# Kernel optimization log

Hardware: AMD Instinct MI355X
Metric: run time of the kernel (lower is better)

The kernel has to match this reference:

```python
import jax, jax.numpy as jnp
import numpy as np

C = 256  # image_channels == mask_channels == output_channels

def setup_inputs() -> dict:
    key = jax.random.key(0)
    ks = jax.random.split(key, 10)
    B, H, W = 16, 48, 48
    s = 0.02
    return {
        "image_feat": jax.random.normal(ks[0], (B, C, H, W), jnp.float32),
        "mask_feat": jax.random.normal(ks[1], (B, C, H, W), jnp.float32),
        "Wq": jax.random.normal(ks[2], (C, C), jnp.float32) * s,
        "bq": jnp.zeros((C,), jnp.float32),
        "Wk": jax.random.normal(ks[3], (C, C), jnp.float32) * s,
        "bk": jnp.zeros((C,), jnp.float32),
        "Wv": jax.random.normal(ks[4], (C, C), jnp.float32) * s,
        "bv": jnp.zeros((C,), jnp.float32),
        "Wo": jax.random.normal(ks[5], (C, C), jnp.float32) * s,
        "bo": jnp.zeros((C,), jnp.float32),
    }

def reference(image_feat, mask_feat, Wq, bq, Wk, bk, Wv, bv, Wo, bo):
    B, Cc, H, W = image_feat.shape
    N = H * W
    img = image_feat.reshape(B, Cc, N)   # [B, C, N]
    msk = mask_feat.reshape(B, Cc, N)
    # 1x1 convs == per-pixel linear over channels
    q = jnp.einsum('oc,bcn->bon', Wq, msk) + bq[None, :, None]
    k = jnp.einsum('oc,bcn->bon', Wk, img) + bk[None, :, None]
    v = jnp.einsum('oc,bcn->bon', Wv, img) + bv[None, :, None]
    scale = Cc ** (-0.5)
    # attn[b, n, m] = <q[:, n], k[:, m]>
    attn = jnp.einsum('bcn,bcm->bnm', q, k) * scale
    attn = jax.nn.softmax(attn, axis=-1)
    # attended[b, c, n] = sum_m v[b, c, m] * attn[b, n, m]
    av = jnp.einsum('bcm,bnm->bcn', v, attn)
    out = jnp.einsum('oc,bcn->bon', Wo, av) + bo[None, :, None]
    return image_feat + out.reshape(B, Cc, H, W)
```

## Files before the change

### kernel.cpp

```cpp
#include <hip/hip_runtime.h>

#define NBATCH 16
#define CCH 256
#define NTOK 2304

typedef __attribute__((ext_vector_type(8))) short bf16x8;
typedef __attribute__((ext_vector_type(4))) short bf16x4v;
typedef __attribute__((ext_vector_type(4))) float f32x4;

__device__ __forceinline__ short f2bf(float x){
  unsigned u = __builtin_bit_cast(unsigned, x);
  u = u + 0x7FFFu + ((u >> 16) & 1u);
  return (short)(u >> 16);
}
__device__ __forceinline__ float bf2f(short h){
  unsigned u = ((unsigned)(unsigned short)h) << 16;
  return __builtin_bit_cast(float, u);
}
__device__ __forceinline__ unsigned char f2fp8(float v){
  return (unsigned char)(__builtin_amdgcn_cvt_pk_fp8_f32(v, v, 0, false) & 0xff);
}

__device__ __forceinline__ void gld_lds16(const void* g, void* l){
  __builtin_amdgcn_global_load_lds((const __attribute__((address_space(1))) void*)g,
                                   (__attribute__((address_space(3))) void*)l, 16, 0, 0);
}

__global__ __launch_bounds__(256) void cw_kernel(const float* __restrict__ Wq, const float* __restrict__ Wk,
                                                 const float* __restrict__ Wv, const float* __restrict__ Wo,
                                                 short* __restrict__ out){
  int idx = blockIdx.x * 256 + threadIdx.x;
  int which = idx >> 14;
  int off = idx & 16383;
  const float* src = which==0 ? Wq : which==1 ? Wk : which==2 ? Wv : Wo;
  float4 v = ((const float4*)src)[off];
  bf16x4v pk = { f2bf(v.x), f2bf(v.y), f2bf(v.z), f2bf(v.w) };
  *(bf16x4v*)(out + ((size_t)which << 16) + ((size_t)off << 2)) = pk;
}

__global__ __launch_bounds__(256) void prep_kernel(const float* __restrict__ img, const float* __restrict__ msk,
                                                   short* __restrict__ imgT, short* __restrict__ mskT){
  int zz = blockIdx.z; int b = zz >> 1; int which = zz & 1;
  const float* src = (which ? msk : img) + (size_t)b * CCH * NTOK;
  short* dst = (which ? mskT : imgT) + (size_t)b * NTOK * CCH;
  int n0 = blockIdx.x * 64, c0 = blockIdx.y * 64;
  __shared__ __align__(16) short tile[64][72];
  int tid = threadIdx.x;
  int r = tid >> 2, g = tid & 3;
  const float* p = src + (size_t)(c0 + r) * NTOK + n0 + 16 * g;
  #pragma unroll
  for (int q4 = 0; q4 < 4; q4++){
    float4 v = *(const float4*)(p + 4 * q4);
    tile[16*g + 4*q4 + 0][r] = f2bf(v.x);
    tile[16*g + 4*q4 + 1][r] = f2bf(v.y);
    tile[16*g + 4*q4 + 2][r] = f2bf(v.z);
    tile[16*g + 4*q4 + 3][r] = f2bf(v.w);
  }
  __syncthreads();
  short* qp = dst + (size_t)(n0 + r) * CCH + c0 + 16 * g;
  *(bf16x8*)qp = *(const bf16x8*)&tile[r][16*g];
  *(bf16x8*)(qp + 8) = *(const bf16x8*)&tile[r][16*g + 8];
}

__device__ __forceinline__ void gemm128(const short* __restrict__ Ablk, const short* __restrict__ Bblk,
                                        short* As, short* Bs, f32x4 (&acc)[4][4]){
  const int tid = threadIdx.x;
  const int l = tid & 63, w = tid >> 6;
  const int l15 = l & 15, lhi = l >> 4;
  const int wi = w >> 1, wj = w & 1;
  const int srow = tid >> 3, scs = tid & 7;
  const f32x4 z4 = {0.f, 0.f, 0.f, 0.f};
  #pragma unroll
  for (int mt = 0; mt < 4; mt++)
    #pragma unroll
    for (int nt = 0; nt < 4; nt++) acc[mt][nt] = z4;

  #pragma unroll 1
  for (int kt = 0; kt < 4; kt++){
    const int k0 = kt * 64;
    bf16x8 ra[4], rb[4];
    #pragma unroll
    for (int p = 0; p < 4; p++){
      const int row = p * 32 + srow;
      ra[p] = *(const bf16x8*)(Ablk + (size_t)row * CCH + k0 + 8 * scs);
      rb[p] = *(const bf16x8*)(Bblk + (size_t)row * CCH + k0 + 8 * scs);
    }
    __syncthreads();
    #pragma unroll
    for (int p = 0; p < 4; p++){
      const int row = p * 32 + srow;
      const int sw = (scs ^ (row & 7)) << 3;
      *(bf16x8*)(As + row * 64 + sw) = ra[p];
      *(bf16x8*)(Bs + row * 64 + sw) = rb[p];
    }
    __syncthreads();
    #pragma unroll
    for (int kk = 0; kk < 2; kk++){
      bf16x8 afr[4], bfr[4];
      #pragma unroll
      for (int mt = 0; mt < 4; mt++){
        const int row = 64 * wi + 16 * mt + l15;
        const int ch = 4 * kk + lhi;
        afr[mt] = *(const bf16x8*)(As + row * 64 + ((ch ^ (row & 7)) << 3));
      }
      #pragma unroll
      for (int nt = 0; nt < 4; nt++){
        const int row = 64 * wj + 16 * nt + l15;
        const int ch = 4 * kk + lhi;
        bfr[nt] = *(const bf16x8*)(Bs + row * 64 + ((ch ^ (row & 7)) << 3));
      }
      #pragma unroll
      for (int mt = 0; mt < 4; mt++)
        #pragma unroll
        for (int nt = 0; nt < 4; nt++)
          acc[mt][nt] = __builtin_amdgcn_mfma_f32_16x16x32_bf16(afr[mt], bfr[nt], acc[mt][nt], 0, 0, 0);
    }
  }
}

__global__ __launch_bounds__(256) void proj_kernel(const short* __restrict__ imgT, const short* __restrict__ mskT,
                                                   const short* __restrict__ Wb,
                                                   const float* __restrict__ bq, const float* __restrict__ bk,
                                                   const float* __restrict__ bv,
                                                   unsigned char* __restrict__ Q8, unsigned char* __restrict__ K8,
                                                   short* __restrict__ Vn){
  __shared__ __align__(16) short As[128 * 64];
  __shared__ __align__(16) short Bs[128 * 64];
  const int b = blockIdx.z, which = blockIdx.y, bx = blockIdx.x;
  const size_t nbT = (size_t)b * NTOK * CCH;
  const short* Ablk; const short* Bblk; const float* bias;
  int ti, tj;
  if (which == 0){
    ti = bx >> 1; tj = bx & 1;
    Ablk = mskT + nbT + (size_t)ti * 128 * CCH;
    Bblk = Wb + (size_t)tj * 128 * CCH;
    bias = bq;
  } else if (which == 1){
    ti = bx >> 1; tj = bx & 1;
    Ablk = imgT + nbT + (size_t)ti * 128 * CCH;
    Bblk = Wb + 65536 + (size_t)tj * 128 * CCH;
    bias = bk;
  } else {
    ti = bx / 18; tj = bx % 18;
    Ablk = Wb + 2 * 65536 + (size_t)ti * 128 * CCH;
    Bblk = imgT + nbT + (size_t)tj * 128 * CCH;
    bias = bv;
  }
  f32x4 acc[4][4];
  gemm128(Ablk, Bblk, As, Bs, acc);
  const int l = threadIdx.x & 63, w = threadIdx.x >> 6;
  const int l15 = l & 15, lhi = l >> 4, wi = w >> 1, wj = w & 1;
  if (which < 2){
    unsigned char* o8 = (which == 0 ? Q8 : K8) + nbT;
    #pragma unroll
    for (int mt = 0; mt < 4; mt++){
      const int i0 = ti * 128 + 64 * wi + 16 * mt + 4 * lhi;
      #pragma unroll
      for (int nt = 0; nt < 4; nt++){
        const int j = tj * 128 + 64 * wj + 16 * nt + l15;
        const float bj = bias[j];
        #pragma unroll
        for (int r = 0; r < 4; r++)
          o8[(size_t)(i0 + r) * CCH + j] = f2fp8(acc[mt][nt][r] + bj);
      }
    }
  } else {
    short* outp = Vn + nbT;
    #pragma unroll
    for (int mt = 0; mt < 4; mt++){
      const int i0 = ti * 128 + 64 * wi + 16 * mt + 4 * lhi;
      #pragma unroll
      for (int nt = 0; nt < 4; nt++){
        const int j = tj * 128 + 64 * wj + 16 * nt + l15;
        #pragma unroll
        for (int r = 0; r < 4; r++)
          outp[(size_t)(i0 + r) * NTOK + j] = f2bf(acc[mt][nt][r] + bias[i0 + r]);
      }
    }
  }
}

__global__ __launch_bounds__(256) void attn_kernel(const unsigned char* __restrict__ Q8,
                                                   const unsigned char* __restrict__ K8,
                                                   const short* __restrict__ Vn,
                                                   short* __restrict__ Opart, float* __restrict__ lsumg){
  const int phys = blockIdx.x;
  const int L = (phys & 7) * 144 + (phys >> 3);
  const int b = L / 72;
  const int rem = L % 72;
  const int half = rem / 36;
  const int q0 = (rem % 36) * 64;
  const int t0 = half * 18;
  const int tid = threadIdx.x, w = tid >> 6, l = tid & 63;
  const int l15 = l & 15, lhi = l >> 4;
  const unsigned char* Qb = Q8 + (size_t)b * NTOK * CCH;
  const unsigned char* Kb = K8 + (size_t)b * NTOK * CCH;
  const short* Vb = Vn + (size_t)b * CCH * NTOK;
  __shared__ __align__(16) unsigned char Ks8[64 * 256];
  __shared__ __align__(16) short P_lds[64 * 64];

  const float SCL = 0.0625f * 1.44269504088896f;
  const int rs2 = (l15 & 7) << 1;

  long qf[8];
  {
    const unsigned char* qrow = Qb + (size_t)(q0 + 16 * w + l15) * CCH + 8 * lhi;
    #pragma unroll
    for (int kk = 0; kk < 8; kk++) qf[kk] = *(const long*)(qrow + 32 * kk);
  }
  const f32x4 z4 = {0.f, 0.f, 0.f, 0.f};
  f32x4 oacc[4][4];
  #pragma unroll
  for (int qt = 0; qt < 4; qt++)
    #pragma unroll
    for (int ct = 0; ct < 4; ct++) oacc[qt][ct] = z4;
  float lpart[4] = {0.f, 0.f, 0.f, 0.f};

#define STAGE_K(M0) do { \
    _Pragma("unroll") \
    for (int r = 0; r < 4; r++){ \
      const int slot = 4 * r + w; \
      const int row = 4 * slot + (l >> 4); \
      const int c16 = (l & 15) ^ (row & 7); \
      gld_lds16(Kb + (size_t)((M0) + row) * CCH + (c16 << 4), &Ks8[slot * 1024]); \
    } } while(0)

  STAGE_K(t0 * 64);

  #pragma unroll 1
  for (int t = t0; t < t0 + 18; t++){
    const int m0 = t * 64;
    __syncthreads();

    bf16x8 vfp[8];
    #pragma unroll
    for (int km = 0; km < 2; km++)
      #pragma unroll
      for (int ct = 0; ct < 4; ct++)
        vfp[4 * km + ct] = *(const bf16x8*)(Vb + (size_t)(64 * w + 16 * ct + l15) * NTOK + m0 + 32 * km + 8 * lhi);

    f32x4 sacc[4] = {z4, z4, z4, z4};
    __builtin_amdgcn_s_setprio(1);
    #pragma unroll
    for (int mjb = 0; mjb < 4; mjb++){
      const int row = 16 * mjb + l15;
      #pragma unroll
      for (int kk = 0; kk < 8; kk++){
        const int c8 = (4 * kk + lhi) ^ rs2;
        long kf = *(const long*)(Ks8 + row * 256 + (c8 << 3));
        sacc[mjb] = __builtin_amdgcn_mfma_f32_16x16x32_fp8_fp8(qf[kk], kf, sacc[mjb], 0, 0, 0);
      }
    }
    __builtin_amdgcn_s_setprio(0);
    #pragma unroll
    for (int mjb = 0; mjb < 4; mjb++)
      #pragma unroll
      for (int r = 0; r < 4; r++){
        float p = exp2f(sacc[mjb][r] * SCL);
        lpart[r] += p;
        const int prow = 16 * w + 4 * lhi + r;
        const int pcol = 16 * mjb + l15;
        P_lds[prow * 64 + ((((pcol >> 3) ^ (prow & 7)) << 3) | (pcol & 7))] = f2bf(p);
      }
    __syncthreads();

    if (t + 1 < t0 + 18) STAGE_K(m0 + 64);

    __builtin_amdgcn_s_setprio(1);
    #pragma unroll
    for (int km = 0; km < 2; km++){
      bf16x8 pf[4];
      #pragma unroll
      for (int qt = 0; qt < 4; qt++){
        const int prow = 16 * qt + l15;
        pf[qt] = *(const bf16x8*)&P_lds[prow * 64 + (((4 * km + lhi) ^ (prow & 7)) << 3)];
      }
      #pragma unroll
      for (int qt = 0; qt < 4; qt++)
        #pragma unroll
        for (int ct = 0; ct < 4; ct++)
          oacc[qt][ct] = __builtin_amdgcn_mfma_f32_16x16x32_bf16(pf[qt], vfp[4 * km + ct], oacc[qt][ct], 0, 0, 0);
    }
    __builtin_amdgcn_s_setprio(0);
  }
#undef STAGE_K

  const size_t hrow = ((size_t)half * NBATCH + b) * NTOK + q0;
  #pragma unroll
  for (int r = 0; r < 4; r++){
    float s = lpart[r];
    s += __shfl_xor(s, 1); s += __shfl_xor(s, 2); s += __shfl_xor(s, 4); s += __shfl_xor(s, 8);
    if (l15 == 0) lsumg[hrow + 16 * w + 4 * lhi + r] = s;
  }
  short* Ob = Opart + hrow * CCH;
  #pragma unroll
  for (int qt = 0; qt < 4; qt++)
    #pragma unroll
    for (int ct = 0; ct < 4; ct++)
      #pragma unroll
      for (int r = 0; r < 4; r++)
        Ob[(size_t)(16 * qt + 4 * lhi + r) * CCH + 64 * w + 16 * ct + l15] = f2bf(oacc[qt][ct][r]);
}

__global__ __launch_bounds__(512, 4) void final_kernel(
    const float* __restrict__ Wo, const float* __restrict__ bo,
    const short* __restrict__ Op, const float* __restrict__ ls,
    const float* __restrict__ img, float* __restrict__ out){
  __shared__ __align__(16) short XL[128 * 72];
  __shared__ __align__(16) short WL[256 * 64];
  const int ti = blockIdx.x, b = blockIdx.y;
  const int n0 = ti * 128;
  const int t = threadIdx.x, wv = t >> 6, l = t & 63;
  const int l15 = l & 15, lhi = l >> 4;
  const int sn = t >> 2, sj = t & 3;
  const int so = t >> 1, sh = t & 1;
  const size_t HS = (size_t)NBATCH * NTOK * CCH;
  const size_t row = (size_t)b * NTOK + n0 + sn;
  const float inv = 1.0f / (ls[row] + ls[(size_t)NBATCH * NTOK + row]);

  const f32x4 z4 = {0.f, 0.f, 0.f, 0.f};
  f32x4 acc[4][4];
  #pragma unroll
  for (int mt = 0; mt < 4; mt++)
    #pragma unroll
    for (int nt = 0; nt < 4; nt++) acc[mt][nt] = z4;

  #pragma unroll 1
  for (int kt = 0; kt < 4; kt++){
    const int c0 = kt * 64;
    bf16x8 a0[2], a1[2];
    #pragma unroll
    for (int j = 0; j < 2; j++){
      const int c = c0 + (2 * sj + j) * 8;
      a0[j] = *(const bf16x8*)(Op + row * CCH + c);
      a1[j] = *(const bf16x8*)(Op + HS + row * CCH + c);
    }
    float4 wreg[8];
    #pragma unroll
    for (int q = 0; q < 8; q++)
      wreg[q] = *(const float4*)(Wo + (size_t)so * CCH + c0 + 32 * sh + 4 * q);
    __syncthreads();
    #pragma unroll
    for (int j = 0; j < 2; j++){
      const int ch = 2 * sj + j;
      bf16x8 cb;
      #pragma unroll
      for (int e = 0; e < 8; e++)
        cb[e] = f2bf((bf2f(a0[j][e]) + bf2f(a1[j][e])) * inv);
      *(bf16x8*)&XL[sn * 72 + ((ch ^ ((sn >> 4) & 7)) << 3)] = cb;
    }
    #pragma unroll
    for (int q = 0; q < 8; q++){
      const int cl = 32 * sh + 4 * q;
      bf16x4v pk = { f2bf(wreg[q].x), f2bf(wreg[q].y), f2bf(wreg[q].z), f2bf(wreg[q].w) };
      *(bf16x4v*)&WL[so * 64 + ((((cl >> 3) ^ (so & 7)) << 3) | (cl & 7))] = pk;
    }
    __syncthreads();
    const int wi = wv & 3, wj = wv >> 2;
    #pragma unroll
    for (int kk = 0; kk < 2; kk++){
      bf16x8 af[4], bf_[4];
      #pragma unroll
      for (int mt = 0; mt < 4; mt++){
        const int o = 64 * wi + 16 * mt + l15;
        af[mt] = *(const bf16x8*)&WL[o * 64 + (((4 * kk + lhi) ^ (o & 7)) << 3)];
      }
      #pragma unroll
      for (int nt = 0; nt < 4; nt++){
        const int n = 64 * wj + 16 * nt + l15;
        bf_[nt] = *(const bf16x8*)&XL[n * 72 + (((4 * kk + lhi) ^ ((n >> 4) & 7)) << 3)];
      }
      #pragma unroll
      for (int mt = 0; mt < 4; mt++)
        #pragma unroll
        for (int nt = 0; nt < 4; nt++)
          acc[mt][nt] = __builtin_amdgcn_mfma_f32_16x16x32_bf16(af[mt], bf_[nt], acc[mt][nt], 0, 0, 0);
    }
  }
  const int wi = wv & 3, wj = wv >> 2;
  const float* imgb = img + (size_t)b * CCH * NTOK;
  float* outb = out + (size_t)b * CCH * NTOK;
  #pragma unroll
  for (int mt = 0; mt < 4; mt++){
    const int ob = 64 * wi + 16 * mt + 4 * lhi;
    #pragma unroll
    for (int nt = 0; nt < 4; nt++){
      const int ng = n0 + 64 * wj + 16 * nt + l15;
      #pragma unroll
      for (int r = 0; r < 4; r++){
        const size_t idx = (size_t)(ob + r) * NTOK + ng;
        outb[idx] = acc[mt][nt][r] + bo[ob + r] + imgb[idx];
      }
    }
  }
}

extern "C" void kernel_launch(void* const* d_in, const int* in_sizes, int n_in,
                              void* d_out, int out_size, void* d_ws, size_t ws_size,
                              hipStream_t stream) {
  const float* img = (const float*)d_in[0];
  const float* msk = (const float*)d_in[1];
  const float* Wq  = (const float*)d_in[2];
  const float* bq  = (const float*)d_in[3];
  const float* Wk  = (const float*)d_in[4];
  const float* bk  = (const float*)d_in[5];
  const float* Wv  = (const float*)d_in[6];
  const float* bv  = (const float*)d_in[7];
  const float* Wo  = (const float*)d_in[8];
  const float* bo  = (const float*)d_in[9];
  float* out = (float*)d_out;

  char* wsb = (char*)d_ws;
  const size_t NE = (size_t)NBATCH * NTOK * CCH;
  short* imgT = (short*)wsb;
  short* mskT = (short*)(wsb + 2 * NE);
  unsigned char* Q8 = (unsigned char*)(wsb + 4 * NE);
  unsigned char* K8 = (unsigned char*)(wsb + 5 * NE);
  short* Vn = (short*)(wsb + 6 * NE);
  short* Wb = (short*)(wsb + 8 * NE);
  float* lsumg = (float*)(wsb + 8 * NE + 4 * 65536 * 2);
  short* Op = (short*)wsb;

  cw_kernel<<<dim3(256), dim3(256), 0, stream>>>(Wq, Wk, Wv, Wo, Wb);
  prep_kernel<<<dim3(36, 4, 32), dim3(256), 0, stream>>>(img, msk, imgT, mskT);
  proj_kernel<<<dim3(36, 3, 16), dim3(256), 0, stream>>>(imgT, mskT, Wb, bq, bk, bv, Q8, K8, Vn);
  attn_kernel<<<dim3(1152), dim3(256), 0, stream>>>(Q8, K8, Vn, Op, lsumg);
  final_kernel<<<dim3(18, 16), dim3(512), 0, stream>>>(Wo, bo, Op, lsumg, img, out);
}
```

Measured before the change: 229.3 us.

## Double-buffer K and P tiles in attention kernel to overlap QK and PV

The attention loop is software-pipelined with two LDS buffers for K and P and two V register sets. The loop is unrolled by two so the PV MFMAs of one tile interleave with the QK MFMAs and softmax of the next, and it needs one barrier per tile instead of two. A launch-bounds occupancy hint of 3 blocks per SM is added. In exchange, LDS use roughly doubles and register pressure rises from the extra V fragments, which could cap occupancy or cause spills.

```diff
diff --git a/kernel.cpp b/kernel.cpp
--- a/kernel.cpp
+++ b/kernel.cpp
@@ -180,10 +180,10 @@
   }
 }
 
-__global__ __launch_bounds__(256) void attn_kernel(const unsigned char* __restrict__ Q8,
-                                                   const unsigned char* __restrict__ K8,
-                                                   const short* __restrict__ Vn,
-                                                   short* __restrict__ Opart, float* __restrict__ lsumg){
+__global__ __launch_bounds__(256, 3) void attn_kernel(const unsigned char* __restrict__ Q8,
+                                                      const unsigned char* __restrict__ K8,
+                                                      const short* __restrict__ Vn,
+                                                      short* __restrict__ Opart, float* __restrict__ lsumg){
   const int phys = blockIdx.x;
   const int L = (phys & 7) * 144 + (phys >> 3);
   const int b = L / 72;
@@ -196,8 +196,8 @@
   const unsigned char* Qb = Q8 + (size_t)b * NTOK * CCH;
   const unsigned char* Kb = K8 + (size_t)b * NTOK * CCH;
   const short* Vb = Vn + (size_t)b * CCH * NTOK;
-  __shared__ __align__(16) unsigned char Ks8[64 * 256];
-  __shared__ __align__(16) short P_lds[64 * 64];
+  __shared__ __align__(16) unsigned char Ks8[2][64 * 256];
+  __shared__ __align__(16) short P_lds[2][64 * 64];
 
   const float SCL = 0.0625f * 1.44269504088896f;
   const int rs2 = (l15 & 7) << 1;
@@ -216,74 +216,92 @@
     for (int ct = 0; ct < 4; ct++) oacc[qt][ct] = z4;
   float lpart[4] = {0.f, 0.f, 0.f, 0.f};
 
-#define STAGE_K(M0) do { \
+#define STAGE_K(BUF, M0) do { \
     _Pragma("unroll") \
     for (int r = 0; r < 4; r++){ \
       const int slot = 4 * r + w; \
       const int row = 4 * slot + (l >> 4); \
       const int c16 = (l & 15) ^ (row & 7); \
-      gld_lds16(Kb + (size_t)((M0) + row) * CCH + (c16 << 4), &Ks8[slot * 1024]); \
+      gld_lds16(Kb + (size_t)((M0) + row) * CCH + (c16 << 4), &Ks8[BUF][slot * 1024]); \
     } } while(0)
 
-  STAGE_K(t0 * 64);
+#define LOAD_V(VFP, M0) do { \
+    _Pragma("unroll") \
+    for (int km = 0; km < 2; km++) \
+      _Pragma("unroll") \
+      for (int ct = 0; ct < 4; ct++) \
+        VFP[4*km+ct] = *(const bf16x8*)(Vb + (size_t)(64*w + 16*ct + l15) * NTOK + (M0) + 32*km + 8*lhi); \
+    } while(0)
+
+#define QK_SM(BUF, PBUF) do { \
+    f32x4 sacc[4] = {z4, z4, z4, z4}; \
+    __builtin_amdgcn_s_setprio(1); \
+    _Pragma("unroll") \
+    for (int mjb = 0; mjb < 4; mjb++){ \
+      const int row = 16 * mjb + l15; \
+      _Pragma("unroll") \
+      for (int kk = 0; kk < 8; kk++){ \
+        const int c8 = (4 * kk + lhi) ^ rs2; \
+        long kf = *(const long*)(&Ks8[BUF][0] + row * 256 + (c8 << 3)); \
+        sacc[mjb] = __builtin_amdgcn_mfma_f32_16x16x32_fp8_fp8(qf[kk], kf, sacc[mjb], 0, 0, 0); \
+      } \
+    } \
+    __builtin_amdgcn_s_setprio(0); \
+    _Pragma("unroll") \
+    for (int mjb = 0; mjb < 4; mjb++) \
+      _Pragma("unroll") \
+      for (int r = 0; r < 4; r++){ \
+        float p = exp2f(sacc[mjb][r] * SCL); \
+        lpart[r] += p; \
+        const int prow = 16 * w + 4 * lhi + r; \
+        const int pcol = 16 * mjb + l15; \
+        P_lds[PBUF][prow * 64 + ((((pcol >> 3) ^ (prow & 7)) << 3) | (pcol & 7))] = f2bf(p); \
+      } \
+    } while(0)
+
+#define PV_STEP(PBUF, VFP) do { \
+    __builtin_amdgcn_s_setprio(1); \
+    _Pragma("unroll") \
+    for (int km = 0; km < 2; km++){ \
+      bf16x8 pf[4]; \
+      _Pragma("unroll") \
+      for (int qt = 0; qt < 4; qt++){ \
+        const int prow = 16 * qt + l15; \
+        pf[qt] = *(const bf16x8*)&P_lds[PBUF][prow * 64 + (((4 * km + lhi) ^ (prow & 7)) << 3)]; \
+      } \
+      _Pragma("unroll") \
+      for (int qt = 0; qt < 4; qt++) \
+        _Pragma("unroll") \
+        for (int ct = 0; ct < 4; ct++) \
+          oacc[qt][ct] = __builtin_amdgcn_mfma_f32_16x16x32_bf16(pf[qt], VFP[4 * km + ct], oacc[qt][ct], 0, 0, 0); \
+    } \
+    __builtin_amdgcn_s_setprio(0); \
+    } while(0)
+
+  bf16x8 vA[8], vB[8];
+  STAGE_K(0, t0 * 64);
+  __syncthreads();
 
   #pragma unroll 1
-  for (int t = t0; t < t0 + 18; t++){
-    const int m0 = t * 64;
-    __syncthreads();
-
-    bf16x8 vfp[8];
-    #pragma unroll
-    for (int km = 0; km < 2; km++)
-      #pragma unroll
-      for (int ct = 0; ct < 4; ct++)
-        vfp[4 * km + ct] = *(const bf16x8*)(Vb + (size_t)(64 * w + 16 * ct + l15) * NTOK + m0 + 32 * km + 8 * lhi);
-
-    f32x4 sacc[4] = {z4, z4, z4, z4};
-    __builtin_amdgcn_s_setprio(1);
-    #pragma unroll
-    for (int mjb = 0; mjb < 4; mjb++){
-      const int row = 16 * mjb + l15;
-      #pragma unroll
-      for (int kk = 0; kk < 8; kk++){
-        const int c8 = (4 * kk + lhi) ^ rs2;
-        long kf = *(const long*)(Ks8 + row * 256 + (c8 << 3));
-        sacc[mjb] = __builtin_amdgcn_mfma_f32_16x16x32_fp8_fp8(qf[kk], kf, sacc[mjb], 0, 0, 0);
-      }
-    }
-    __builtin_amdgcn_s_setprio(0);
-    #pragma unroll
-    for (int mjb = 0; mjb < 4; mjb++)
-      #pragma unroll
-      for (int r = 0; r < 4; r++){
-        float p = exp2f(sacc[mjb][r] * SCL);
-        lpart[r] += p;
-        const int prow = 16 * w + 4 * lhi + r;
-        const int pcol = 16 * mjb + l15;
-        P_lds[prow * 64 + ((((pcol >> 3) ^ (prow & 7)) << 3) | (pcol & 7))] = f2bf(p);
-      }
-    __syncthreads();
-
-    if (t + 1 < t0 + 18) STAGE_K(m0 + 64);
-
-    __builtin_amdgcn_s_setprio(1);
-    #pragma unroll
-    for (int km = 0; km < 2; km++){
-      bf16x8 pf[4];
-      #pragma unroll
-      for (int qt = 0; qt < 4; qt++){
-        const int prow = 16 * qt + l15;
-        pf[qt] = *(const bf16x8*)&P_lds[prow * 64 + (((4 * km + lhi) ^ (prow & 7)) << 3)];
-      }
-      #pragma unroll
-      for (int qt = 0; qt < 4; qt++)
-        #pragma unroll
-        for (int ct = 0; ct < 4; ct++)
-          oacc[qt][ct] = __builtin_amdgcn_mfma_f32_16x16x32_bf16(pf[qt], vfp[4 * km + ct], oacc[qt][ct], 0, 0, 0);
-    }
-    __builtin_amdgcn_s_setprio(0);
-  }
+  for (int u = 0; u < 9; u++){
+    const int tA = t0 + 2 * u;
+    const int tB = tA + 1;
+    STAGE_K(1, tB * 64);
+    LOAD_V(vA, tA * 64);
+    if (u > 0) PV_STEP(1, vB);
+    QK_SM(0, 0);
+    __syncthreads();
+    if (u < 8) STAGE_K(0, (tB + 1) * 64);
+    LOAD_V(vB, tB * 64);
+    PV_STEP(0, vA);
+    QK_SM(1, 1);
+    __syncthreads();
+  }
+  PV_STEP(1, vB);
 #undef STAGE_K
+#undef LOAD_V
+#undef QK_SM
+#undef PV_STEP
 
   const size_t hrow = ((size_t)half * NBATCH + b) * NTOK + q0;
   #pragma unroll
```

New measurement: 414.7 us. 1.81x slower.
